# Performance work log

Hardware: AMD Instinct MI355X
Metric: run time of the kernel (lower is better)

Reference implementation:

```python
import jax, jax.numpy as jnp
import numpy as np

B, T, D, FF, H, K = 8, 1024, 512, 2048, 8, 15
HD = D // H  # key_dim = d_model // num_heads


def _ln(x, g, b):
    # keras LayerNormalization default epsilon = 1e-3
    m = jnp.mean(x, axis=-1, keepdims=True)
    v = jnp.var(x, axis=-1, keepdims=True)
    return (x - m) * jax.lax.rsqrt(v + 1e-3) * g + b


def setup_inputs() -> dict:
    key = jax.random.key(0)
    ks = iter(jax.random.split(key, 64))

    def rn(shape, s=0.02):
        return jax.random.normal(next(ks), shape, jnp.float32) * s

    p = {}
    p['x'] = jax.random.normal(next(ks), (B, T, D), jnp.float32)
    # ff_pre: LN -> Dense(FF, relu) -> Dense(D)
    p['g1'] = jnp.ones((D,), jnp.float32); p['b1'] = jnp.zeros((D,), jnp.float32)
    p['Wff1'] = rn((D, FF)); p['bff1'] = jnp.zeros((FF,), jnp.float32)
    p['Wff2'] = rn((FF, D)); p['bff2'] = jnp.zeros((D,), jnp.float32)
    # attention norm + MHA projections (keras EinsumDense shapes)
    p['ga'] = jnp.ones((D,), jnp.float32); p['ba'] = jnp.zeros((D,), jnp.float32)
    p['Wq'] = rn((D, H, HD)); p['bq'] = jnp.zeros((H, HD), jnp.float32)
    p['Wk'] = rn((D, H, HD)); p['bk'] = jnp.zeros((H, HD), jnp.float32)
    p['Wv'] = rn((D, H, HD)); p['bv'] = jnp.zeros((H, HD), jnp.float32)
    p['Wo'] = rn((H, HD, D)); p['bo'] = jnp.zeros((D,), jnp.float32)
    # conv branch: LN -> pointwise conv (2D, gelu) -> depthwise conv(k=15) -> BN -> swish -> pointwise conv (D)
    p['gc'] = jnp.ones((D,), jnp.float32); p['bc'] = jnp.zeros((D,), jnp.float32)
    p['Wcp'] = rn((D, 2 * D)); p['bcp'] = jnp.zeros((2 * D,), jnp.float32)
    p['dwk'] = rn((K, 1, 2 * D)); p['dwb'] = jnp.zeros((2 * D,), jnp.float32)
    p['bn_g'] = jnp.ones((2 * D,), jnp.float32); p['bn_b'] = jnp.zeros((2 * D,), jnp.float32)
    p['bn_m'] = jnp.zeros((2 * D,), jnp.float32)
    p['bn_v'] = jnp.ones((2 * D,), jnp.float32)
    p['Wco'] = rn((2 * D, D)); p['bco'] = jnp.zeros((D,), jnp.float32)
    # ff_post
    p['g2'] = jnp.ones((D,), jnp.float32); p['b2'] = jnp.zeros((D,), jnp.float32)
    p['Wf1'] = rn((D, FF)); p['bf1'] = jnp.zeros((FF,), jnp.float32)
    p['Wf2'] = rn((FF, D)); p['bf2'] = jnp.zeros((D,), jnp.float32)
    return p


def reference(x, g1, b1, Wff1, bff1, Wff2, bff2, ga, ba, Wq, bq, Wk, bk, Wv, bv, Wo, bo, gc, bc, Wcp, bcp, dwk, dwb, bn_g, bn_b, bn_m, bn_v, Wco, bco, g2, b2, Wf1, bf1, Wf2, bf2):
    # Macaron FFN (pre), half-step residual applied later
    x_ff = jnp.maximum(_ln(x, g1, b1) @ Wff1 + bff1, 0.0) @ Wff2 + bff2

    # causal multi-head self-attention (cache=None path)
    a = _ln(x, ga, ba)
    q = jnp.einsum('btd,dhk->bthk', a, Wq) + bq
    k = jnp.einsum('btd,dhk->bthk', a, Wk) + bk
    v = jnp.einsum('btd,dhk->bthk', a, Wv) + bv
    scores = jnp.einsum('bqhd,bkhd->bhqk', q, k) / jnp.sqrt(jnp.float32(HD))
    causal = jnp.tril(jnp.ones((T, T), bool))  # [T,T]
    scores = jnp.where(causal, scores, jnp.float32(-1e9))
    w = jax.nn.softmax(scores, axis=-1)
    ctx = jnp.einsum('bhqk,bkhd->bqhd', w, v)
    attn = jnp.einsum('bqhd,hdo->bqo', ctx, Wo) + bo

    x = x + 0.5 * x_ff + attn

    # convolution module: pointwise(gelu) -> causal left-pad -> depthwise -> BN(inference) -> swish -> pointwise
    c = jax.nn.gelu(_ln(x, gc, bc) @ Wcp + bcp, approximate=False)
    c = jnp.pad(c, ((0, 0), (K - 1, 0), (0, 0)))  # causal pad
    c = jax.lax.conv_general_dilated(
        c, dwk, window_strides=(1,), padding='VALID',
        dimension_numbers=('NWC', 'WIO', 'NWC'), feature_group_count=2 * D) + dwb
    c = (c - bn_m) * jax.lax.rsqrt(bn_v + 1e-3) * bn_g + bn_b
    c = c * jax.nn.sigmoid(c)  # swish
    c = c @ Wco + bco
    x = x + c

    # post FFN (full residual)
    x = x + (jnp.maximum(_ln(x, g2, b2) @ Wf1 + bf1, 0.0) @ Wf2 + bf2)
    return x
```

## Files before the change

kernel.cpp:

```cpp
#include <hip/hip_runtime.h>
#include <hip/hip_bf16.h>
#include <math.h>

#define BB 8
#define TT 1024
#define DD 512
#define FFD 2048
#define HH 8
#define HDD 64
#define KW 15
#define MR (BB*TT)
#define QKVN 1536

typedef __attribute__((ext_vector_type(8))) short short8;
typedef __attribute__((ext_vector_type(4))) short short4v;
typedef __attribute__((ext_vector_type(4))) float f32x4;
typedef __hip_bfloat16 bf16;

__device__ __forceinline__ float bf2f(unsigned u16) {
    return __uint_as_float(u16 << 16);
}

__device__ __forceinline__ void async_copy16(const void* g, void* l) {
    __builtin_amdgcn_global_load_lds(
        (const __attribute__((address_space(1))) void*)g,
        (__attribute__((address_space(3))) void*)l, 16, 0, 0);
}

__device__ __forceinline__ float gelu_exact(float v) {
    return 0.5f * v * (1.0f + erff(v * 0.70710678118654752f));
}

struct PrepPack {
    const float* src[10];
    bf16*        dst[10];
    int          K[10];
    int          lgNT[10];
    float        scale[10];
    int          off[10];
    const float* bq; const float* bk; const float* bv;
    float*       bdst;
    const float* x;
    const float* g1; const float* b1; const float* ga; const float* ba;
    bf16* o1; bf16* o2;
};

__global__ __launch_bounds__(256) void prep_kernel(PrepPack P) {
    __shared__ alignas(16) bf16 T[64][72];
    const int bid = blockIdx.x;
    if (bid == 1536) {
        #pragma unroll
        for (int it = 0; it < 6; ++it) {
            int i = it * 256 + threadIdx.x;
            float v = i < 512 ? P.bq[i] * 0.125f
                              : (i < 1024 ? P.bk[i - 512] : P.bv[i - 1024]);
            P.bdst[i] = v;
        }
        return;
    }
    if (bid > 1536) {
        int wave = ((bid - 1537) * 256 + (int)threadIdx.x) >> 6;
        int lane = threadIdx.x & 63;
        const float* row = P.x + (size_t)wave * DD;
        float4 v0 = ((const float4*)row)[lane];
        float4 v1 = ((const float4*)row)[64 + lane];
        float s  = v0.x + v0.y + v0.z + v0.w + v1.x + v1.y + v1.z + v1.w;
        float ss = v0.x*v0.x + v0.y*v0.y + v0.z*v0.z + v0.w*v0.w
                 + v1.x*v1.x + v1.y*v1.y + v1.z*v1.z + v1.w*v1.w;
        #pragma unroll
        for (int off = 32; off >= 1; off >>= 1) {
            s  += __shfl_xor(s,  off, 64);
            ss += __shfl_xor(ss, off, 64);
        }
        float mean = s * (1.0f / DD);
        float var  = ss * (1.0f / DD) - mean * mean;
        float r    = rsqrtf(var + 1e-3f);
        float n0x = (v0.x - mean) * r, n0y = (v0.y - mean) * r,
              n0z = (v0.z - mean) * r, n0w = (v0.w - mean) * r;
        float n1x = (v1.x - mean) * r, n1y = (v1.y - mean) * r,
              n1z = (v1.z - mean) * r, n1w = (v1.w - mean) * r;
        {
            float4 g0 = ((const float4*)P.g1)[lane];
            float4 gg = ((const float4*)P.g1)[64 + lane];
            float4 b0 = ((const float4*)P.b1)[lane];
            float4 bb = ((const float4*)P.b1)[64 + lane];
            alignas(8) bf16 o0[4], o1[4];
            o0[0] = __float2bfloat16(n0x * g0.x + b0.x);
            o0[1] = __float2bfloat16(n0y * g0.y + b0.y);
            o0[2] = __float2bfloat16(n0z * g0.z + b0.z);
            o0[3] = __float2bfloat16(n0w * g0.w + b0.w);
            o1[0] = __float2bfloat16(n1x * gg.x + bb.x);
            o1[1] = __float2bfloat16(n1y * gg.y + bb.y);
            o1[2] = __float2bfloat16(n1z * gg.z + bb.z);
            o1[3] = __float2bfloat16(n1w * gg.w + bb.w);
            bf16* orow = P.o1 + (size_t)wave * DD;
            *(short4v*)(orow + lane * 4)       = *(const short4v*)o0;
            *(short4v*)(orow + 256 + lane * 4) = *(const short4v*)o1;
        }
        {
            float4 g0 = ((const float4*)P.ga)[lane];
            float4 gg = ((const float4*)P.ga)[64 + lane];
            float4 b0 = ((const float4*)P.ba)[lane];
            float4 bb = ((const float4*)P.ba)[64 + lane];
            alignas(8) bf16 o0[4], o1[4];
            o0[0] = __float2bfloat16(n0x * g0.x + b0.x);
            o0[1] = __float2bfloat16(n0y * g0.y + b0.y);
            o0[2] = __float2bfloat16(n0z * g0.z + b0.z);
            o0[3] = __float2bfloat16(n0w * g0.w + b0.w);
            o1[0] = __float2bfloat16(n1x * gg.x + bb.x);
            o1[1] = __float2bfloat16(n1y * gg.y + bb.y);
            o1[2] = __float2bfloat16(n1z * gg.z + bb.z);
            o1[3] = __float2bfloat16(n1w * gg.w + bb.w);
            bf16* orow = P.o2 + (size_t)wave * DD;
            *(short4v*)(orow + lane * 4)       = *(const short4v*)o0;
            *(short4v*)(orow + 256 + lane * 4) = *(const short4v*)o1;
        }
        return;
    }
    int e = 0;
    #pragma unroll
    for (int i = 1; i < 10; ++i) e = (bid >= P.off[i]) ? i : e;
    const float* W  = P.src[e];
    bf16*        Wt = P.dst[e];
    const int    K  = P.K[e];
    const int    lg = P.lgNT[e];
    const float  scale = P.scale[e];
    const int local = bid - P.off[e];
    const int bx = local & ((1 << lg) - 1);
    const int by = local >> lg;
    const int k0 = by * 64;
    const int n0 = bx * 64;
    const int N  = (1 << lg) * 64;
    const int tid = threadIdx.x;
    #pragma unroll
    for (int it = 0; it < 4; ++it) {
        int lin = it * 256 + tid;
        int kl  = lin >> 4;
        int nq  = (lin & 15) * 4;
        float4 v = *(const float4*)(W + (size_t)(k0 + kl) * N + n0 + nq);
        T[nq + 0][kl] = __float2bfloat16(v.x * scale);
        T[nq + 1][kl] = __float2bfloat16(v.y * scale);
        T[nq + 2][kl] = __float2bfloat16(v.z * scale);
        T[nq + 3][kl] = __float2bfloat16(v.w * scale);
    }
    __syncthreads();
    #pragma unroll
    for (int it = 0; it < 4; ++it) {
        int lin = it * 256 + tid;
        int nl  = lin >> 4;
        int kq  = (lin & 15) * 4;
        *(short4v*)(Wt + (size_t)(n0 + nl) * K + k0 + kq) = *(const short4v*)&T[nl][kq];
    }
}

__global__ __launch_bounds__(256) void ln_kernel(const float* __restrict__ x,
                                                 const float* __restrict__ g,
                                                 const float* __restrict__ b,
                                                 bf16* __restrict__ out) {
    int wave = (blockIdx.x * blockDim.x + threadIdx.x) >> 6;
    int lane = threadIdx.x & 63;
    if (wave >= MR) return;
    const float* row = x + (size_t)wave * DD;
    float4 v0 = ((const float4*)row)[lane];
    float4 v1 = ((const float4*)row)[64 + lane];
    float s  = v0.x + v0.y + v0.z + v0.w + v1.x + v1.y + v1.z + v1.w;
    float ss = v0.x*v0.x + v0.y*v0.y + v0.z*v0.z + v0.w*v0.w
             + v1.x*v1.x + v1.y*v1.y + v1.z*v1.z + v1.w*v1.w;
    #pragma unroll
    for (int off = 32; off >= 1; off >>= 1) {
        s  += __shfl_xor(s,  off, 64);
        ss += __shfl_xor(ss, off, 64);
    }
    float mean = s * (1.0f / DD);
    float var  = ss * (1.0f / DD) - mean * mean;
    float r    = rsqrtf(var + 1e-3f);
    float4 g0 = ((const float4*)g)[lane];
    float4 g1 = ((const float4*)g)[64 + lane];
    float4 b0 = ((const float4*)b)[lane];
    float4 b1 = ((const float4*)b)[64 + lane];
    alignas(8) bf16 o0[4], o1[4];
    o0[0] = __float2bfloat16((v0.x - mean) * r * g0.x + b0.x);
    o0[1] = __float2bfloat16((v0.y - mean) * r * g0.y + b0.y);
    o0[2] = __float2bfloat16((v0.z - mean) * r * g0.z + b0.z);
    o0[3] = __float2bfloat16((v0.w - mean) * r * g0.w + b0.w);
    o1[0] = __float2bfloat16((v1.x - mean) * r * g1.x + b1.x);
    o1[1] = __float2bfloat16((v1.y - mean) * r * g1.y + b1.y);
    o1[2] = __float2bfloat16((v1.z - mean) * r * g1.z + b1.z);
    o1[3] = __float2bfloat16((v1.w - mean) * r * g1.w + b1.w);
    bf16* orow = out + (size_t)wave * DD;
    *(short4v*)(orow + lane * 4)       = *(const short4v*)o0;
    *(short4v*)(orow + 256 + lane * 4) = *(const short4v*)o1;
}

template<int BN, int OP, int RESMODE, int OUTMODE>
__global__ __launch_bounds__(256) void bgemm_kernel(
    const bf16* __restrict__ A,
    const bf16* __restrict__ Bt,
    const float* __restrict__ bias,
    const float* __restrict__ res1,
    const bf16* __restrict__ res2,
    float s2, float oscale,
    void* __restrict__ Cout,
    int N, int Kd, int nxb)
{
    constexpr int NT = BN / 32;
    __shared__ alignas(16) bf16 As[128][64];
    __shared__ alignas(16) bf16 Bs[BN][64];
    const int tid  = threadIdx.x;
    const int w    = tid >> 6;
    const int lane = tid & 63;
    const int quad = lane >> 4;
    const int l16  = lane & 15;
    const int wm   = w >> 1, wn = w & 1;

    const int flat = blockIdx.x;
    const int c8   = flat & 7;
    const int j    = flat >> 3;
    const int jy   = j / nxb;
    const int m0   = (c8 * 8 + jy) * 128;
    const int n0   = (j - jy * nxb) * BN;

    const int srow = lane >> 3;
    const int scol = ((lane & 7) ^ srow) * 8;

    const bf16* Ap = A  + (size_t)(m0 + w * 32 + srow) * Kd + scol;
    const bf16* Bp = Bt + (size_t)(n0 + w * (BN / 4) + srow) * Kd + scol;

    f32x4 acc[4][NT] = {};

    for (int k0 = 0; k0 < Kd; k0 += 64) {
        #pragma unroll
        for (int i = 0; i < 4; ++i)
            async_copy16(Ap + (size_t)(i * 8) * Kd + k0, &As[w * 32 + i * 8][0]);
        #pragma unroll
        for (int i = 0; i < BN / 32; ++i)
            async_copy16(Bp + (size_t)(i * 8) * Kd + k0, &Bs[w * (BN / 4) + i * 8][0]);
        __syncthreads();
        #pragma unroll
        for (int ks = 0; ks < 2; ++ks) {
            short8 af[4], bfr[NT];
            #pragma unroll
            for (int mt = 0; mt < 4; ++mt) {
                const int row = wm * 64 + mt * 16 + l16;
// ... 14 lines not shown
                        af[mt], bfr[nt], acc[mt][nt], 0, 0, 0);
        }
        __syncthreads();
    }

    const int crow0 = m0 + wm * 64 + quad * 4;
    const int ccol0 = n0 + wn * (BN / 2) + l16;
    #pragma unroll
    for (int nt = 0; nt < NT; ++nt) {
        const int col = ccol0 + nt * 16;
        const float bv = bias[col];
        #pragma unroll
        for (int mt = 0; mt < 4; ++mt) {
            #pragma unroll
            for (int r = 0; r < 4; ++r) {
                const int row = crow0 + mt * 16 + r;
                const size_t off = (size_t)row * N + col;
                float o = acc[mt][nt][r] + bv;
                if (OP == 1)      o = fmaxf(o, 0.f);
                else if (OP == 2) o = gelu_exact(o);
                if (RESMODE >= 1) o += res1[off];
                if (RESMODE == 2) o += s2 * __bfloat162float(res2[off]);
                if (OUTMODE == 0) ((float*)Cout)[off] = o;
                else              ((bf16*)Cout)[off]  = __float2bfloat16(o * oscale);
            }
        }
    }
}

__global__ __launch_bounds__(256) void ffqkv_kernel(
    const bf16* __restrict__ lnb, const bf16* __restrict__ lnab,
    const bf16* __restrict__ Wff1t, const bf16* __restrict__ Wqkvt,
    const float* __restrict__ bff1, const float* __restrict__ bqkv,
    bf16* __restrict__ bigb, bf16* __restrict__ qkvb, bf16* __restrict__ Vtb)
{
    __shared__ alignas(16) bf16 As[128][64];
    __shared__ alignas(16) bf16 Bs[128][64];
    const int tid  = threadIdx.x;
    const int w    = tid >> 6;
    const int lane = tid & 63;
    const int quad = lane >> 4;
    const int l16  = lane & 15;
    const int wm   = w >> 1, wn = w & 1;

    const bool jobq = blockIdx.x >= 1024;
    const int  flat = jobq ? (int)blockIdx.x - 1024 : (int)blockIdx.x;
    const int  nxb  = jobq ? 12 : 16;
    const int  N    = jobq ? QKVN : FFD;
    const bf16* A   = jobq ? lnab : lnb;
    const bf16* Bt  = jobq ? Wqkvt : Wff1t;
    const float* bias = jobq ? bqkv : bff1;

    const int c8 = flat & 7;
    const int j  = flat >> 3;
    const int jy = j / nxb;
    const int m0 = (c8 * 8 + jy) * 128;
    const int n0 = (j - jy * nxb) * 128;

    const int srow = lane >> 3;
    const int scol = ((lane & 7) ^ srow) * 8;

    const bf16* Ap = A  + (size_t)(m0 + w * 32 + srow) * DD + scol;
    const bf16* Bp = Bt + (size_t)(n0 + w * 32 + srow) * DD + scol;

    f32x4 acc[4][4] = {};

    for (int k0 = 0; k0 < DD; k0 += 64) {
        #pragma unroll
        for (int i = 0; i < 4; ++i) {
            async_copy16(Ap + (size_t)(i * 8) * DD + k0, &As[w * 32 + i * 8][0]);
            async_copy16(Bp + (size_t)(i * 8) * DD + k0, &Bs[w * 32 + i * 8][0]);
        }
        __syncthreads();
        #pragma unroll
// ... 17 lines not shown
                for (int nt = 0; nt < 4; ++nt)
                    acc[mt][nt] = __builtin_amdgcn_mfma_f32_16x16x32_bf16(
                        af[mt], bfr[nt], acc[mt][nt], 0, 0, 0);
        }
        __syncthreads();
    }

    const int crow0 = m0 + wm * 64 + quad * 4;
    const int ccol0 = n0 + wn * 64 + l16;
    #pragma unroll
    for (int nt = 0; nt < 4; ++nt) {
        const int col = ccol0 + nt * 16;
        const float bv = bias[col];
        #pragma unroll
        for (int mt = 0; mt < 4; ++mt) {
            if (jobq) {
                alignas(8) bf16 o4[4];
                #pragma unroll
                for (int r = 0; r < 4; ++r)
                    o4[r] = __float2bfloat16(acc[mt][nt][r] + bv);
                if (col < 1024) {
                    #pragma unroll
                    for (int r = 0; r < 4; ++r)
                        qkvb[(size_t)(crow0 + mt * 16 + r) * QKVN + col] = o4[r];
                } else {
                    const int dg   = col - 1024;
                    const int rowt = crow0 + mt * 16;
                    const int bb   = rowt >> 10, t0 = rowt & 1023;
                    const int bh2  = bb * 8 + (dg >> 6), d = dg & 63;
                    *(short4v*)(Vtb + ((size_t)bh2 * 64 + d) * TT + t0) =
                        *(const short4v*)o4;
                }
            } else {
                #pragma unroll
                for (int r = 0; r < 4; ++r) {
                    const float o = fmaxf(acc[mt][nt][r] + bv, 0.f);
                    bigb[(size_t)(crow0 + mt * 16 + r) * FFD + col] =
                        __float2bfloat16(o);
                }
            }
        }
    }
}

__global__ __launch_bounds__(256) void ff2attn_kernel(
    const bf16* __restrict__ QKV, const bf16* __restrict__ Vt,
    bf16* __restrict__ ctx,
    const bf16* __restrict__ bigb, const bf16* __restrict__ Wff2t,
    const float* __restrict__ bff2, bf16* __restrict__ xffb)
{
    __shared__ alignas(16) bf16 smem[16384];
    const int tid  = threadIdx.x;
    const int w    = tid >> 6;
    const int lane = tid & 63;
    const int quad = lane >> 4;
    const int l16  = lane & 15;

    if (blockIdx.x < 512) {
        typedef bf16 (*tile_t)[64][64];
        tile_t Ks = (tile_t)smem;
        tile_t Vs = (tile_t)(smem + 2 * 64 * 64);
        const int bh = blockIdx.x & 63;
        const int bi = 7 - ((int)blockIdx.x >> 6);
        const int b = bh >> 3, h = bh & 7;

        const bf16* Qg = QKV + (size_t)(b * TT) * QKVN + h * 64;
        const bf16* Kg = QKV + (size_t)(b * TT) * QKVN + 512 + h * 64;
        const bf16* Vg = Vt  + (size_t)bh * 64 * TT;

        const int qL = bi * 128 + w * 16;
        const int qH = qL + 64;
        short8 qfL0 = *(const short8*)(Qg + (size_t)(qL + l16) * QKVN + quad * 8);
        short8 qfL1 = *(const short8*)(Qg + (size_t)(qL + l16) * QKVN + 32 + quad * 8);
        short8 qfH0 = *(const short8*)(Qg + (size_t)(qH + l16) * QKVN + quad * 8);
        short8 qfH1 = *(const short8*)(Qg + (size_t)(qH + l16) * QKVN + 32 + quad * 8);

        const int sgrow  = lane >> 3;
        const int sgchnk = lane & 7;

        f32x4 caccL[4] = {}, caccH[4] = {};
        float lL = 0.f, lH = 0.f;
        const int prow_base = ((l16 >> 2) << 3) + (l16 & 3);
        const int smax = 2 * bi + 1;

        #pragma unroll
        for (int i = 0; i < 2; ++i) {
            const int rowbase = w * 8 + i * 32;
            const int row = rowbase + sgrow;
            const int fR = (row & 3) | (((row >> 3) & 1) << 2);
            const int sc = sgchnk ^ fR;
            async_copy16(Kg + (size_t)row * QKVN + sc * 8, &Ks[0][rowbase][0]);
// ... 90 lines not shown
            #pragma unroll
            for (int g = 0; g < 4; ++g) {
                const int vrow = g * 16 + l16;
                const int fR = (vrow & 3) | (((vrow >> 3) & 1) << 2);
                short8 va = *(const short8*)&Vs[buf][vrow][(quad ^ fR) * 8];
                short8 vb = *(const short8*)&Vs[buf][vrow][((4 + quad) ^ fR) * 8];
                caccH[g] = __builtin_amdgcn_mfma_f32_16x16x32_bf16(va, pfH0, caccH[g], 0, 0, 0);
                caccH[g] = __builtin_amdgcn_mfma_f32_16x16x32_bf16(vb, pfH1, caccH[g], 0, 0, 0);
                if (doL) {
                    caccL[g] = __builtin_amdgcn_mfma_f32_16x16x32_bf16(va, pfL0, caccL[g], 0, 0, 0);
                    caccL[g] = __builtin_amdgcn_mfma_f32_16x16x32_bf16(vb, pfL1, caccL[g], 0, 0, 0);
                }
            }
            buf ^= 1;
        }

        lL += __shfl_xor(lL, 16, 64);
        lL += __shfl_xor(lL, 32, 64);
        lH += __shfl_xor(lH, 16, 64);
        lH += __shfl_xor(lH, 32, 64);
        const float invL = 1.0f / lL;
        const float invH = 1.0f / lH;

        bf16* CbL = ctx + (size_t)(b * TT + qL + l16) * DD + h * 64;
        bf16* CbH = ctx + (size_t)(b * TT + qH + l16) * DD + h * 64;
        #pragma unroll
        for (int g = 0; g < 4; ++g) {
            alignas(8) bf16 oL[4], oH[4];
            #pragma unroll
            for (int r = 0; r < 4; ++r) {
                oL[r] = __float2bfloat16(caccL[g][r] * invL);
                oH[r] = __float2bfloat16(caccH[g][r] * invH);
            }
            *(short4v*)(CbL + g * 16 + quad * 4) = *(const short4v*)oL;
            *(short4v*)(CbH + g * 16 + quad * 4) = *(const short4v*)oH;
        }
    } else {
        typedef bf16 (*row_t)[64];
        row_t As = (row_t)smem;
        row_t Bs = (row_t)(smem + 128 * 64);
        const int wm = w >> 1, wn = w & 1;

        const int flat = (int)blockIdx.x - 512;
        const int c8 = flat & 7;
        const int j  = flat >> 3;
        const int jy = j >> 3;
        const int m0 = (c8 * 8 + jy) * 128;
        const int n0 = (j & 7) * 64;

        const int srow = lane >> 3;
        const int scol = ((lane & 7) ^ srow) * 8;

        const bf16* Ap = bigb  + (size_t)(m0 + w * 32 + srow) * FFD + scol;
        const bf16* Bp = Wff2t + (size_t)(n0 + w * 16 + srow) * FFD + scol;

        f32x4 acc[4][2] = {};

        for (int k0 = 0; k0 < FFD; k0 += 64) {
            #pragma unroll
            for (int i = 0; i < 4; ++i)
                async_copy16(Ap + (size_t)(i * 8) * FFD + k0, &As[w * 32 + i * 8][0]);
            #pragma unroll
            for (int i = 0; i < 2; ++i)
                async_copy16(Bp + (size_t)(i * 8) * FFD + k0, &Bs[w * 16 + i * 8][0]);
            __syncthreads();
            #pragma unroll
            for (int ks = 0; ks < 2; ++ks) {
                short8 af[4], bfr[2];
                #pragma unroll
                for (int mt = 0; mt < 4; ++mt) {
                    const int row = wm * 64 + mt * 16 + l16;
                    const int c   = ((ks * 4 + quad) ^ (row & 7)) * 16;
                    af[mt] = *(const short8*)((const char*)&As[row][0] + c);
                }
                #pragma unroll
                for (int nt = 0; nt < 2; ++nt) {
                    const int col = wn * 32 + nt * 16 + l16;
                    const int c   = ((ks * 4 + quad) ^ (col & 7)) * 16;
                    bfr[nt] = *(const short8*)((const char*)&Bs[col][0] + c);
                }
                #pragma unroll
                for (int mt = 0; mt < 4; ++mt)
                    #pragma unroll
                    for (int nt = 0; nt < 2; ++nt)
                        acc[mt][nt] = __builtin_amdgcn_mfma_f32_16x16x32_bf16(
                            af[mt], bfr[nt], acc[mt][nt], 0, 0, 0);
            }
            __syncthreads();
        }

        const int crow0 = m0 + wm * 64 + quad * 4;
        const int ccol0 = n0 + wn * 32 + l16;
        #pragma unroll
        for (int nt = 0; nt < 2; ++nt) {
            const int col = ccol0 + nt * 16;
            const float bv = bff2[col];
            #pragma unroll
            for (int mt = 0; mt < 4; ++mt)
                #pragma unroll
                for (int r = 0; r < 4; ++r) {
                    const int row = crow0 + mt * 16 + r;
                    xffb[(size_t)row * DD + col] =
                        __float2bfloat16(acc[mt][nt][r] + bv);
                }
        }
    }
}

__global__ __launch_bounds__(256) void dwconv_kernel(const bf16* __restrict__ c1,
                                                     const float* __restrict__ dwk,
                                                     const float* __restrict__ dwb,
                                                     const float* __restrict__ bn_g,
                                                     const float* __restrict__ bn_b,
                                                     const float* __restrict__ bn_m,
                                                     const float* __restrict__ bn_v,
                                                     bf16* __restrict__ out) {
    const int C2 = 2 * DD;
    const int lin = blockIdx.x * 256 + threadIdx.x;
    const int chp = lin & 511;
    const int ch  = chp << 1;
    const int tch = lin >> 9;
    const int row0 = tch << 3;
    const int t0   = row0 & (TT - 1);

    float w0[KW], w1[KW];
    #pragma unroll
    for (int i = 0; i < KW; ++i) {
        w0[i] = dwk[i * C2 + ch];
        w1[i] = dwk[i * C2 + ch + 1];
    }
    const float a0 = rsqrtf(bn_v[ch] + 1e-3f) * bn_g[ch];
    const float a1 = rsqrtf(bn_v[ch + 1] + 1e-3f) * bn_g[ch + 1];
    const float c0 = (dwb[ch] - bn_m[ch]) * a0 + bn_b[ch];
    const float c1v = (dwb[ch + 1] - bn_m[ch + 1]) * a1 + bn_b[ch + 1];

    float x0[22], x1[22];
    if (t0 >= KW - 1) {
        #pragma unroll
        for (int i = 0; i < 22; ++i) {
            unsigned u = *(const unsigned*)(c1 + (size_t)(row0 - (KW - 1) + i) * C2 + ch);
            x0[i] = bf2f(u & 0xffff);
            x1[i] = bf2f(u >> 16);
        }
    } else {
        #pragma unroll
        for (int i = 0; i < 22; ++i) {
            unsigned u = 0;
            if (t0 - (KW - 1) + i >= 0)
                u = *(const unsigned*)(c1 + (size_t)(row0 - (KW - 1) + i) * C2 + ch);
            x0[i] = bf2f(u & 0xffff);
            x1[i] = bf2f(u >> 16);
        }
    }

    #pragma unroll
    for (int j = 0; j < 8; ++j) {
        float s0 = 0.f, s1 = 0.f;
        #pragma unroll
        for (int i = 0; i < KW; ++i) {
            s0 += x0[j + i] * w0[i];
            s1 += x1[j + i] * w1[i];
        }
        s0 = s0 * a0 + c0;
        s1 = s1 * a1 + c1v;
        s0 = s0 / (1.f + __expf(-s0));
        s1 = s1 / (1.f + __expf(-s1));
        alignas(4) bf16 ob[2] = {__float2bfloat16(s0), __float2bfloat16(s1)};
        *(unsigned*)(out + (size_t)(row0 + j) * C2 + ch) = *(const unsigned*)ob;
    }
}

extern "C" void kernel_launch(void* const* d_in, const int* in_sizes, int n_in,
                              void* d_out, int out_size, void* d_ws, size_t ws_size,
                              hipStream_t stream) {
    const float* x    = (const float*)d_in[0];
    const float* g1   = (const float*)d_in[1];
    const float* b1   = (const float*)d_in[2];
    const float* Wff1 = (const float*)d_in[3];
    const float* bff1 = (const float*)d_in[4];
    const float* Wff2 = (const float*)d_in[5];
    const float* bff2 = (const float*)d_in[6];
    const float* ga   = (const float*)d_in[7];
    const float* ba   = (const float*)d_in[8];
    const float* Wq   = (const float*)d_in[9];
    const float* bq   = (const float*)d_in[10];
    const float* Wk   = (const float*)d_in[11];
    const float* bk   = (const float*)d_in[12];
    const float* Wv   = (const float*)d_in[13];
    const float* bv   = (const float*)d_in[14];
    const float* Wo   = (const float*)d_in[15];
    const float* bo   = (const float*)d_in[16];
    const float* gc   = (const float*)d_in[17];
    const float* bc   = (const float*)d_in[18];
    const float* Wcp  = (const float*)d_in[19];
    const float* bcp  = (const float*)d_in[20];
    const float* dwk  = (const float*)d_in[21];
    const float* dwb  = (const float*)d_in[22];
    const float* bn_g = (const float*)d_in[23];
    const float* bn_b = (const float*)d_in[24];
    const float* bn_m = (const float*)d_in[25];
    const float* bn_v = (const float*)d_in[26];
    const float* Wco  = (const float*)d_in[27];
    const float* bco  = (const float*)d_in[28];
    const float* g2   = (const float*)d_in[29];
    const float* b2   = (const float*)d_in[30];
    const float* Wf1  = (const float*)d_in[31];
    const float* bf1  = (const float*)d_in[32];
    const float* Wf2  = (const float*)d_in[33];
    const float* bf2  = (const float*)d_in[34];

    float* out = (float*)d_out;

    char* p = (char*)d_ws;
    bf16* lnb   = (bf16*)p;  p += (size_t)MR * DD * 2;
    bf16* lnab  = (bf16*)p;  p += (size_t)MR * DD * 2;
    bf16* qkvb  = (bf16*)p;  p += (size_t)MR * QKVN * 2;
    bf16* Vtb   = (bf16*)p;  p += (size_t)MR * DD * 2;
    bf16* ctxb  = (bf16*)p;  p += (size_t)MR * DD * 2;
    bf16* xffb  = (bf16*)p;  p += (size_t)MR * DD * 2;
    bf16* bigb  = (bf16*)p;  p += (size_t)MR * FFD * 2;
    bf16* c2b   = (bf16*)p;  p += (size_t)MR * 1024 * 2;
    bf16* Wff1t = (bf16*)p;  p += (size_t)FFD * DD * 2;
    bf16* Wff2t = (bf16*)p;  p += (size_t)DD * FFD * 2;
    bf16* Wqkvt = (bf16*)p;  p += (size_t)QKVN * DD * 2;
    bf16* Wot   = (bf16*)p;  p += (size_t)DD * DD * 2;
    bf16* Wcpt  = (bf16*)p;  p += (size_t)1024 * DD * 2;
    bf16* Wcot  = (bf16*)p;  p += (size_t)DD * 1024 * 2;
    bf16* Wf1t  = (bf16*)p;  p += (size_t)FFD * DD * 2;
    bf16* Wf2t  = (bf16*)p;  p += (size_t)DD * FFD * 2;
    float* bqkv = (float*)p; p += QKVN * 4;

    dim3 blk(256);

    PrepPack P;
    auto set = [&](int i, const float* s, bf16* d, int K, int N, float sc, int off) {
        P.src[i] = s; P.dst[i] = d; P.K[i] = K; P.scale[i] = sc; P.off[i] = off;
        int nt = N / 64, lg = 0; while ((1 << lg) < nt) ++lg; P.lgNT[i] = lg;
    };
    set(0, Wff1, Wff1t, DD,  FFD, 1.f,    0);
    set(1, Wff2, Wff2t, FFD, DD,  1.f,    256);
    set(2, Wq,   Wqkvt,                DD, DD, 0.125f, 512);
    set(3, Wk,   Wqkvt + (size_t)512 * DD,  DD, DD, 1.f, 576);
    set(4, Wv,   Wqkvt + (size_t)1024 * DD, DD, DD, 1.f, 640);
    set(5, Wo,   Wot,   DD,  DD,  1.f,    704);
    set(6, Wcp,  Wcpt,  DD,  1024, 1.f,   768);
    set(7, Wco,  Wcot,  1024, DD, 1.f,    896);
    set(8, Wf1,  Wf1t,  DD,  FFD, 1.f,    1024);
    set(9, Wf2,  Wf2t,  FFD, DD,  1.f,    1280);
    P.bq = bq; P.bk = bk; P.bv = bv; P.bdst = bqkv;
    P.x = x; P.g1 = g1; P.b1 = b1; P.ga = ga; P.ba = ba;
    P.o1 = lnb; P.o2 = lnab;

    prep_kernel<<<dim3(1537 + MR / 4), blk, 0, stream>>>(P);
    ffqkv_kernel<<<dim3(1024 + 768), blk, 0, stream>>>(
        lnb, lnab, Wff1t, Wqkvt, bff1, bqkv, bigb, qkvb, Vtb);
    ff2attn_kernel<<<dim3(1024), blk, 0, stream>>>(
        qkvb, Vtb, ctxb, bigb, Wff2t, bff2, xffb);
    bgemm_kernel<64, 0, 2, 0><<<dim3(8 * 64), blk, 0, stream>>>(
        ctxb, Wot, bo, x, xffb, 0.5f, 1.f, out, DD, DD, 8);
    ln_kernel<<<dim3(MR / 4), blk, 0, stream>>>(out, gc, bc, lnb);
    bgemm_kernel<128, 2, 0, 1><<<dim3(8 * 64), blk, 0, stream>>>(
        lnb, Wcpt, bcp, nullptr, nullptr, 0.f, 1.f, bigb, 1024, DD, 8);
    dwconv_kernel<<<dim3(MR * 512 / 8 / 256), blk, 0, stream>>>(
        bigb, dwk, dwb, bn_g, bn_b, bn_m, bn_v, c2b);
    bgemm_kernel<64, 0, 1, 0><<<dim3(8 * 64), blk, 0, stream>>>(
        c2b, Wcot, bco, out, nullptr, 0.f, 1.f, out, DD, 1024, 8);
    ln_kernel<<<dim3(MR / 4), blk, 0, stream>>>(out, g2, b2, lnb);
    bgemm_kernel<128, 1, 0, 1><<<dim3(16 * 64), blk, 0, stream>>>(
        lnb, Wf1t, bf1, nullptr, nullptr, 0.f, 1.f, bigb, FFD, DD, 16);
    bgemm_kernel<64, 0, 1, 0><<<dim3(8 * 64), blk, 0, stream>>>(
        bigb, Wf2t, bf2, out, nullptr, 0.f, 1.f, out, DD, FFD, 8);
}
```

Measured before the change: 385.7 us.

## Fuse all stages into one persistent megakernel with software grid barriers

New measurement: 890.9 us. +131.0%, slower.

```diff
diff --git a/kernel.cpp b/kernel.cpp
--- a/kernel.cpp
+++ b/kernel.cpp
@@ -11,6 +11,7 @@
 #define KW 15
 #define MR (BB*TT)
 #define QKVN 1536
+#define NBLK 512
 
 typedef __attribute__((ext_vector_type(8))) short short8;
 typedef __attribute__((ext_vector_type(4))) short short4v;
@@ -31,135 +32,42 @@
     return 0.5f * v * (1.0f + erff(v * 0.70710678118654752f));
 }
 
-struct PrepPack {
-    const float* src[10];
-    bf16*        dst[10];
-    int          K[10];
-    int          lgNT[10];
-    float        scale[10];
-    int          off[10];
-    const float* bq; const float* bk; const float* bv;
-    float*       bdst;
-    const float* x;
-    const float* g1; const float* b1; const float* ga; const float* ba;
-    bf16* o1; bf16* o2;
+__device__ __forceinline__ void grid_barrier(unsigned* cnt, int phase) {
+    __syncthreads();
+    if (threadIdx.x == 0) {
+        __threadfence();
+        atomicAdd(cnt, 1u);
+        const unsigned target = (unsigned)phase * NBLK;
+        while (atomicAdd(cnt, 0u) < target)
+            __builtin_amdgcn_s_sleep(8);
+        __threadfence();
+    }
+    __syncthreads();
+}
+
+struct MegaArgs {
+    const float* wsrc[10];
+    bf16*        wdst[10];
+    int          wK[10];
+    int          wlgNT[10];
+    float        wscale[10];
+    int          woff[10];
+    const float *bq, *bk, *bv;
+    float*       bqkv;
+    const float *x;
+    const float *g1, *b1, *ga, *ba, *gc, *bc, *g2, *b2;
+    const float *bff1, *bff2, *bo, *bcp, *bco, *bf1, *bf2;
+    const float *dwk, *dwb, *bn_g, *bn_b, *bn_m, *bn_v;
+    const bf16 *Wff1t, *Wff2t, *Wqkvt, *Wot, *Wcpt, *Wcot, *Wf1t, *Wf2t;
+    bf16 *lnb, *lnab, *qkvb, *Vtb, *ctxb, *xffb, *bigb, *c2b;
+    float* out;
+    unsigned* bar;
 };
 
-__global__ __launch_bounds__(256) void prep_kernel(PrepPack P) {
-    __shared__ alignas(16) bf16 T[64][72];
-    const int bid = blockIdx.x;
-    if (bid == 1536) {
-        #pragma unroll
-        for (int it = 0; it < 6; ++it) {
-            int i = it * 256 + threadIdx.x;
-            float v = i < 512 ? P.bq[i] * 0.125f
-                              : (i < 1024 ? P.bk[i - 512] : P.bv[i - 1024]);
-            P.bdst[i] = v;
-        }
-        return;
-    }
-    if (bid > 1536) {
-        int wave = ((bid - 1537) * 256 + (int)threadIdx.x) >> 6;
-        int lane = threadIdx.x & 63;
-        const float* row = P.x + (size_t)wave * DD;
-        float4 v0 = ((const float4*)row)[lane];
-        float4 v1 = ((const float4*)row)[64 + lane];
-        float s  = v0.x + v0.y + v0.z + v0.w + v1.x + v1.y + v1.z + v1.w;
-        float ss = v0.x*v0.x + v0.y*v0.y + v0.z*v0.z + v0.w*v0.w
-                 + v1.x*v1.x + v1.y*v1.y + v1.z*v1.z + v1.w*v1.w;
-        #pragma unroll
-        for (int off = 32; off >= 1; off >>= 1) {
-            s  += __shfl_xor(s,  off, 64);
-            ss += __shfl_xor(ss, off, 64);
-        }
-        float mean = s * (1.0f / DD);
-        float var  = ss * (1.0f / DD) - mean * mean;
-        float r    = rsqrtf(var + 1e-3f);
-        float n0x = (v0.x - mean) * r, n0y = (v0.y - mean) * r,
-              n0z = (v0.z - mean) * r, n0w = (v0.w - mean) * r;
-        float n1x = (v1.x - mean) * r, n1y = (v1.y - mean) * r,
-              n1z = (v1.z - mean) * r, n1w = (v1.w - mean) * r;
-        {
-            float4 g0 = ((const float4*)P.g1)[lane];
-            float4 gg = ((const float4*)P.g1)[64 + lane];
-            float4 b0 = ((const float4*)P.b1)[lane];
-            float4 bb = ((const float4*)P.b1)[64 + lane];
-            alignas(8) bf16 o0[4], o1[4];
-            o0[0] = __float2bfloat16(n0x * g0.x + b0.x);
-            o0[1] = __float2bfloat16(n0y * g0.y + b0.y);
-            o0[2] = __float2bfloat16(n0z * g0.z + b0.z);
-            o0[3] = __float2bfloat16(n0w * g0.w + b0.w);
-            o1[0] = __float2bfloat16(n1x * gg.x + bb.x);
-            o1[1] = __float2bfloat16(n1y * gg.y + bb.y);
-            o1[2] = __float2bfloat16(n1z * gg.z + bb.z);
-            o1[3] = __float2bfloat16(n1w * gg.w + bb.w);
-            bf16* orow = P.o1 + (size_t)wave * DD;
-            *(short4v*)(orow + lane * 4)       = *(const short4v*)o0;
-            *(short4v*)(orow + 256 + lane * 4) = *(const short4v*)o1;
-        }
-        {
-            float4 g0 = ((const float4*)P.ga)[lane];
-            float4 gg = ((const float4*)P.ga)[64 + lane];
-            float4 b0 = ((const float4*)P.ba)[lane];
-            float4 bb = ((const float4*)P.ba)[64 + lane];
-            alignas(8) bf16 o0[4], o1[4];
-            o0[0] = __float2bfloat16(n0x * g0.x + b0.x);
-            o0[1] = __float2bfloat16(n0y * g0.y + b0.y);
-            o0[2] = __float2bfloat16(n0z * g0.z + b0.z);
-            o0[3] = __float2bfloat16(n0w * g0.w + b0.w);
-            o1[0] = __float2bfloat16(n1x * gg.x + bb.x);
-            o1[1] = __float2bfloat16(n1y * gg.y + bb.y);
-            o1[2] = __float2bfloat16(n1z * gg.z + bb.z);
-            o1[3] = __float2bfloat16(n1w * gg.w + bb.w);
-            bf16* orow = P.o2 + (size_t)wave * DD;
-            *(short4v*)(orow + lane * 4)       = *(const short4v*)o0;
-            *(short4v*)(orow + 256 + lane * 4) = *(const short4v*)o1;
-        }
-        return;
-    }
-    int e = 0;
-    #pragma unroll
-    for (int i = 1; i < 10; ++i) e = (bid >= P.off[i]) ? i : e;
-    const float* W  = P.src[e];
-    bf16*        Wt = P.dst[e];
-    const int    K  = P.K[e];
-    const int    lg = P.lgNT[e];
-    const float  scale = P.scale[e];
-    const int local = bid - P.off[e];
-    const int bx = local & ((1 << lg) - 1);
-    const int by = local >> lg;
-    const int k0 = by * 64;
-    const int n0 = bx * 64;
-    const int N  = (1 << lg) * 64;
-    const int tid = threadIdx.x;
-    #pragma unroll
-    for (int it = 0; it < 4; ++it) {
-        int lin = it * 256 + tid;
-        int kl  = lin >> 4;
-        int nq  = (lin & 15) * 4;
-        float4 v = *(const float4*)(W + (size_t)(k0 + kl) * N + n0 + nq);
-        T[nq + 0][kl] = __float2bfloat16(v.x * scale);
-        T[nq + 1][kl] = __float2bfloat16(v.y * scale);
-        T[nq + 2][kl] = __float2bfloat16(v.z * scale);
-        T[nq + 3][kl] = __float2bfloat16(v.w * scale);
-    }
-    __syncthreads();
-    #pragma unroll
-    for (int it = 0; it < 4; ++it) {
-        int lin = it * 256 + tid;
-        int nl  = lin >> 4;
-        int kq  = (lin & 15) * 4;
-        *(short4v*)(Wt + (size_t)(n0 + nl) * K + k0 + kq) = *(const short4v*)&T[nl][kq];
-    }
-}
-
-__global__ __launch_bounds__(256) void ln_kernel(const float* __restrict__ x,
-                                                 const float* __restrict__ g,
-                                                 const float* __restrict__ b,
-                                                 bf16* __restrict__ out) {
-    int wave = (blockIdx.x * blockDim.x + threadIdx.x) >> 6;
+__device__ __forceinline__ void dev_ln(int job, const float* x, const float* g,
+                                       const float* b, bf16* out) {
+    int wave = (job * 256 + (int)threadIdx.x) >> 6;
     int lane = threadIdx.x & 63;
-    if (wave >= MR) return;
     const float* row = x + (size_t)wave * DD;
     float4 v0 = ((const float4*)row)[lane];
     float4 v1 = ((const float4*)row)[64 + lane];
@@ -192,20 +100,124 @@
     *(short4v*)(orow + 256 + lane * 4) = *(const short4v*)o1;
 }
 
+__device__ __forceinline__ void dev_prep(int bid, const MegaArgs& A, bf16* smem) {
+    if (bid == 1536) {
+        #pragma unroll
+        for (int it = 0; it < 6; ++it) {
+            int i = it * 256 + threadIdx.x;
+            float v = i < 512 ? A.bq[i] * 0.125f
+                              : (i < 1024 ? A.bk[i - 512] : A.bv[i - 1024]);
+            A.bqkv[i] = v;
+        }
+        return;
+    }
+    if (bid > 1536) {
+        int wave = ((bid - 1537) * 256 + (int)threadIdx.x) >> 6;
+        int lane = threadIdx.x & 63;
+        const float* row = A.x + (size_t)wave * DD;
+        float4 v0 = ((const float4*)row)[lane];
+        float4 v1 = ((const float4*)row)[64 + lane];
+        float s  = v0.x + v0.y + v0.z + v0.w + v1.x + v1.y + v1.z + v1.w;
+        float ss = v0.x*v0.x + v0.y*v0.y + v0.z*v0.z + v0.w*v0.w
+                 + v1.x*v1.x + v1.y*v1.y + v1.z*v1.z + v1.w*v1.w;
+        #pragma unroll
+        for (int off = 32; off >= 1; off >>= 1) {
+            s  += __shfl_xor(s,  off, 64);
+            ss += __shfl_xor(ss, off, 64);
+        }
+        float mean = s * (1.0f / DD);
+        float var  = ss * (1.0f / DD) - mean * mean;
+        float r    = rsqrtf(var + 1e-3f);
+        float n0x = (v0.x - mean) * r, n0y = (v0.y - mean) * r,
+              n0z = (v0.z - mean) * r, n0w = (v0.w - mean) * r;
+        float n1x = (v1.x - mean) * r, n1y = (v1.y - mean) * r,
+              n1z = (v1.z - mean) * r, n1w = (v1.w - mean) * r;
+        {
+            float4 g0 = ((const float4*)A.g1)[lane];
+            float4 gg = ((const float4*)A.g1)[64 + lane];
+            float4 b0 = ((const float4*)A.b1)[lane];
+            float4 bb = ((const float4*)A.b1)[64 + lane];
+            alignas(8) bf16 o0[4], o1[4];
+            o0[0] = __float2bfloat16(n0x * g0.x + b0.x);
+            o0[1] = __float2bfloat16(n0y * g0.y + b0.y);
+            o0[2] = __float2bfloat16(n0z * g0.z + b0.z);
+            o0[3] = __float2bfloat16(n0w * g0.w + b0.w);
+            o1[0] = __float2bfloat16(n1x * gg.x + bb.x);
+            o1[1] = __float2bfloat16(n1y * gg.y + bb.y);
+            o1[2] = __float2bfloat16(n1z * gg.z + bb.z);
+            o1[3] = __float2bfloat16(n1w * gg.w + bb.w);
+            bf16* orow = A.lnb + (size_t)wave * DD;
+            *(short4v*)(orow + lane * 4)       = *(const short4v*)o0;
+            *(short4v*)(orow + 256 + lane * 4) = *(const short4v*)o1;
+        }
+        {
+            float4 g0 = ((const float4*)A.ga)[lane];
+            float4 gg = ((const float4*)A.ga)[64 + lane];
+            float4 b0 = ((const float4*)A.ba)[lane];
+            float4 bb = ((const float4*)A.ba)[64 + lane];
+            alignas(8) bf16 o0[4], o1[4];
+            o0[0] = __float2bfloat16(n0x * g0.x + b0.x);
+            o0[1] = __float2bfloat16(n0y * g0.y + b0.y);
+            o0[2] = __float2bfloat16(n0z * g0.z + b0.z);
+            o0[3] = __float2bfloat16(n0w * g0.w + b0.w);
+            o1[0] = __float2bfloat16(n1x * gg.x + bb.x);
+            o1[1] = __float2bfloat16(n1y * gg.y + bb.y);
+            o1[2] = __float2bfloat16(n1z * gg.z + bb.z);
+            o1[3] = __float2bfloat16(n1w * gg.w + bb.w);
+            bf16* orow = A.lnab + (size_t)wave * DD;
+            *(short4v*)(orow + lane * 4)       = *(const short4v*)o0;
+            *(short4v*)(orow + 256 + lane * 4) = *(const short4v*)o1;
+        }
+        return;
+    }
+    bf16 (*T)[72] = (bf16(*)[72])smem;
+    int e = 0;
+    #pragma unroll
+    for (int i = 1; i < 10; ++i) e = (bid >= A.woff[i]) ? i : e;
+    const float* W  = A.wsrc[e];
+    bf16*        Wt = A.wdst[e];
+    const int    K  = A.wK[e];
+    const int    lg = A.wlgNT[e];
+    const float  scale = A.wscale[e];
+    const int local = bid - A.woff[e];
+    const int bx = local & ((1 << lg) - 1);
+    const int by = local >> lg;
+    const int k0 = by * 64;
+    const int n0 = bx * 64;
+    const int N  = (1 << lg) * 64;
+    const int tid = threadIdx.x;
+    #pragma unroll
+    for (int it = 0; it < 4; ++it) {
+        int lin = it * 256 + tid;
+        int kl  = lin >> 4;
+        int nq  = (lin & 15) * 4;
+        float4 v = *(const float4*)(W + (size_t)(k0 + kl) * N + n0 + nq);
+        T[nq + 0][kl] = __float2bfloat16(v.x * scale);
+        T[nq + 1][kl] = __float2bfloat16(v.y * scale);
+        T[nq + 2][kl] = __float2bfloat16(v.z * scale);
+        T[nq + 3][kl] = __float2bfloat16(v.w * scale);
+    }
+    __syncthreads();
+    #pragma unroll
+    for (int it = 0; it < 4; ++it) {
+        int lin = it * 256 + tid;
+        int nl  = lin >> 4;
+        int kq  = (lin & 15) * 4;
+        *(short4v*)(Wt + (size_t)(n0 + nl) * K + k0 + kq) = *(const short4v*)&T[nl][kq];
+    }
+    __syncthreads();
+}
+
 template<int BN, int OP, int RESMODE, int OUTMODE>
-__global__ __launch_bounds__(256) void bgemm_kernel(
-    const bf16* __restrict__ A,
-    const bf16* __restrict__ Bt,
-    const float* __restrict__ bias,
-    const float* __restrict__ res1,
-    const bf16* __restrict__ res2,
-    float s2, float oscale,
-    void* __restrict__ Cout,
+__device__ __forceinline__ void dev_gemm(int flat, bf16* smem,
+    const bf16* __restrict__ A, const bf16* __restrict__ Bt,
+    const float* __restrict__ bias, const float* __restrict__ res1,
+    const bf16* __restrict__ res2, float s2, void* __restrict__ Cout,
     int N, int Kd, int nxb)
 {
     constexpr int NT = BN / 32;
-    __shared__ alignas(16) bf16 As[128][64];
-    __shared__ alignas(16) bf16 Bs[BN][64];
+    bf16 (*As)[64] = (bf16(*)[64])smem;
+    bf16 (*Bs)[64] = (bf16(*)[64])(smem + 128 * 64);
     const int tid  = threadIdx.x;
     const int w    = tid >> 6;
     const int lane = tid & 63;
@@ -213,12 +225,11 @@
     const int l16  = lane & 15;
     const int wm   = w >> 1, wn = w & 1;
 
-    const int flat = blockIdx.x;
-    const int c8   = flat & 7;
-    const int j    = flat >> 3;
-    const int jy   = j / nxb;
-    const int m0   = (c8 * 8 + jy) * 128;
-    const int n0   = (j - jy * nxb) * BN;
+    const int c8 = flat & 7;
+    const int j  = flat >> 3;
+    const int jy = j / nxb;
+    const int m0 = (c8 * 8 + jy) * 128;
+    const int n0 = (j - jy * nxb) * BN;
 
     const int srow = lane >> 3;
     const int scol = ((lane & 7) ^ srow) * 8;
@@ -279,20 +290,15 @@
                 if (RESMODE >= 1) o += res1[off];
                 if (RESMODE == 2) o += s2 * __bfloat162float(res2[off]);
                 if (OUTMODE == 0) ((float*)Cout)[off] = o;
-                else              ((bf16*)Cout)[off]  = __float2bfloat16(o * oscale);
-            }
-        }
-    }
-}
-
-__global__ __launch_bounds__(256) void ffqkv_kernel(
-    const bf16* __restrict__ lnb, const bf16* __restrict__ lnab,
-    const bf16* __restrict__ Wff1t, const bf16* __restrict__ Wqkvt,
-    const float* __restrict__ bff1, const float* __restrict__ bqkv,
-    bf16* __restrict__ bigb, bf16* __restrict__ qkvb, bf16* __restrict__ Vtb)
-{
-    __shared__ alignas(16) bf16 As[128][64];
-    __shared__ alignas(16) bf16 Bs[128][64];
+                else              ((bf16*)Cout)[off]  = __float2bfloat16(o);
+            }
+        }
+    }
+}
+
+__device__ __forceinline__ void dev_ffqkv(int job, bf16* smem, const MegaArgs& Ar) {
+    bf16 (*As)[64] = (bf16(*)[64])smem;
+    bf16 (*Bs)[64] = (bf16(*)[64])(smem + 128 * 64);
     const int tid  = threadIdx.x;
     const int w    = tid >> 6;
     const int lane = tid & 63;
@@ -300,13 +306,13 @@
     const int l16  = lane & 15;
     const int wm   = w >> 1, wn = w & 1;
 
-    const bool jobq = blockIdx.x >= 1024;
-    const int  flat = jobq ? (int)blockIdx.x - 1024 : (int)blockIdx.x;
+    const bool jobq = job >= 1024;
+    const int  flat = jobq ? job - 1024 : job;
     const int  nxb  = jobq ? 12 : 16;
     const int  N    = jobq ? QKVN : FFD;
-    const bf16* A   = jobq ? lnab : lnb;
-    const bf16* Bt  = jobq ? Wqkvt : Wff1t;
-    const float* bias = jobq ? bqkv : bff1;
+    const bf16* A   = jobq ? Ar.lnab : Ar.lnb;
+    const bf16* Bt  = jobq ? Ar.Wqkvt : Ar.Wff1t;
+    const float* bias = jobq ? Ar.bqkv : Ar.bff1;
 
     const int c8 = flat & 7;
     const int j  = flat >> 3;
@@ -370,20 +376,20 @@
                 if (col < 1024) {
                     #pragma unroll
                     for (int r = 0; r < 4; ++r)
-                        qkvb[(size_t)(crow0 + mt * 16 + r) * QKVN + col] = o4[r];
+                        Ar.qkvb[(size_t)(crow0 + mt * 16 + r) * QKVN + col] = o4[r];
                 } else {
                     const int dg   = col - 1024;
                     const int rowt = crow0 + mt * 16;
                     const int bb   = rowt >> 10, t0 = rowt & 1023;
                     const int bh2  = bb * 8 + (dg >> 6), d = dg & 63;
-                    *(short4v*)(Vtb + ((size_t)bh2 * 64 + d) * TT + t0) =
+                    *(short4v*)(Ar.Vtb + ((size_t)bh2 * 64 + d) * TT + t0) =
                         *(const short4v*)o4;
                 }
             } else {
                 #pragma unroll
                 for (int r = 0; r < 4; ++r) {
                     const float o = fmaxf(acc[mt][nt][r] + bv, 0.f);
-                    bigb[(size_t)(crow0 + mt * 16 + r) * FFD + col] =
+                    Ar.bigb[(size_t)(crow0 + mt * 16 + r) * FFD + col] =
                         __float2bfloat16(o);
                 }
             }
@@ -391,30 +397,24 @@
     }
 }
 
-__global__ __launch_bounds__(256) void ff2attn_kernel(
-    const bf16* __restrict__ QKV, const bf16* __restrict__ Vt,
-    bf16* __restrict__ ctx,
-    const bf16* __restrict__ bigb, const bf16* __restrict__ Wff2t,
-    const float* __restrict__ bff2, bf16* __restrict__ xffb)
-{
-    __shared__ alignas(16) bf16 smem[16384];
+__device__ __forceinline__ void dev_ff2attn(int job, bf16* smem, const MegaArgs& Ar) {
     const int tid  = threadIdx.x;
     const int w    = tid >> 6;
     const int lane = tid & 63;
     const int quad = lane >> 4;
     const int l16  = lane & 15;
 
-    if (blockIdx.x < 512) {
+    if (job < 512) {
         typedef bf16 (*tile_t)[64][64];
         tile_t Ks = (tile_t)smem;
         tile_t Vs = (tile_t)(smem + 2 * 64 * 64);
-        const int bh = blockIdx.x & 63;
-        const int bi = 7 - ((int)blockIdx.x >> 6);
+        const int bh = job & 63;
+        const int bi = 7 - (job >> 6);
         const int b = bh >> 3, h = bh & 7;
 
-        const bf16* Qg = QKV + (size_t)(b * TT) * QKVN + h * 64;
-        const bf16* Kg = QKV + (size_t)(b * TT) * QKVN + 512 + h * 64;
-        const bf16* Vg = Vt  + (size_t)bh * 64 * TT;
+        const bf16* Qg = Ar.qkvb + (size_t)(b * TT) * QKVN + h * 64;
+        const bf16* Kg = Ar.qkvb + (size_t)(b * TT) * QKVN + 512 + h * 64;
+        const bf16* Vg = Ar.Vtb  + (size_t)bh * 64 * TT;
 
         const int qL = bi * 128 + w * 16;
         const int qH = qL + 64;
@@ -551,8 +551,8 @@
         const float invL = 1.0f / lL;
         const float invH = 1.0f / lH;
 
-        bf16* CbL = ctx + (size_t)(b * TT + qL + l16) * DD + h * 64;
-        bf16* CbH = ctx + (size_t)(b * TT + qH + l16) * DD + h * 64;
+        bf16* CbL = Ar.ctxb + (size_t)(b * TT + qL + l16) * DD + h * 64;
+        bf16* CbH = Ar.ctxb + (size_t)(b * TT + qH + l16) * DD + h * 64;
         #pragma unroll
         for (int g = 0; g < 4; ++g) {
             alignas(8) bf16 oL[4], oH[4];
@@ -564,13 +564,13 @@
             *(short4v*)(CbL + g * 16 + quad * 4) = *(const short4v*)oL;
             *(short4v*)(CbH + g * 16 + quad * 4) = *(const short4v*)oH;
         }
+        __syncthreads();
     } else {
-        typedef bf16 (*row_t)[64];
-        row_t As = (row_t)smem;
-        row_t Bs = (row_t)(smem + 128 * 64);
+        bf16 (*As)[64] = (bf16(*)[64])smem;
+        bf16 (*Bs)[64] = (bf16(*)[64])(smem + 128 * 64);
         const int wm = w >> 1, wn = w & 1;
 
-        const int flat = (int)blockIdx.x - 512;
+        const int flat = job - 512;
         const int c8 = flat & 7;
         const int j  = flat >> 3;
         const int jy = j >> 3;
@@ -580,8 +580,8 @@
         const int srow = lane >> 3;
         const int scol = ((lane & 7) ^ srow) * 8;
 
-        const bf16* Ap = bigb  + (size_t)(m0 + w * 32 + srow) * FFD + scol;
-        const bf16* Bp = Wff2t + (size_t)(n0 + w * 16 + srow) * FFD + scol;
+        const bf16* Ap = Ar.bigb  + (size_t)(m0 + w * 32 + srow) * FFD + scol;
+        const bf16* Bp = Ar.Wff2t + (size_t)(n0 + w * 16 + srow) * FFD + scol;
 
         f32x4 acc[4][2] = {};
 
@@ -623,45 +623,39 @@
         #pragma unroll
         for (int nt = 0; nt < 2; ++nt) {
             const int col = ccol0 + nt * 16;
-            const float bv = bff2[col];
+            const float bv = Ar.bff2[col];
             #pragma unroll
             for (int mt = 0; mt < 4; ++mt)
                 #pragma unroll
                 for (int r = 0; r < 4; ++r) {
                     const int row = crow0 + mt * 16 + r;
-                    xffb[(size_t)row * DD + col] =
+                    Ar.xffb[(size_t)row * DD + col] =
                         __float2bfloat16(acc[mt][nt][r] + bv);
                 }
         }
     }
 }
 
-__global__ __launch_bounds__(256) void dwconv_kernel(const bf16* __restrict__ c1,
-                                                     const float* __restrict__ dwk,
-                                                     const float* __restrict__ dwb,
-                                                     const float* __restrict__ bn_g,
-                                                     const float* __restrict__ bn_b,
-                                                     const float* __restrict__ bn_m,
-                                                     const float* __restrict__ bn_v,
-                                                     bf16* __restrict__ out) {
+__device__ __forceinline__ void dev_dwconv(int job, const MegaArgs& A) {
     const int C2 = 2 * DD;
-    const int lin = blockIdx.x * 256 + threadIdx.x;
+    const int lin = job * 256 + threadIdx.x;
     const int chp = lin & 511;
     const int ch  = chp << 1;
     const int tch = lin >> 9;
     const int row0 = tch << 3;
     const int t0   = row0 & (TT - 1);
+    const bf16* c1 = A.bigb;
 
     float w0[KW], w1[KW];
     #pragma unroll
     for (int i = 0; i < KW; ++i) {
-        w0[i] = dwk[i * C2 + ch];
-        w1[i] = dwk[i * C2 + ch + 1];
-    }
-    const float a0 = rsqrtf(bn_v[ch] + 1e-3f) * bn_g[ch];
-    const float a1 = rsqrtf(bn_v[ch + 1] + 1e-3f) * bn_g[ch + 1];
-    const float c0 = (dwb[ch] - bn_m[ch]) * a0 + bn_b[ch];
-    const float c1v = (dwb[ch + 1] - bn_m[ch + 1]) * a1 + bn_b[ch + 1];
+        w0[i] = A.dwk[i * C2 + ch];
+        w1[i] = A.dwk[i * C2 + ch + 1];
+    }
+    const float a0 = rsqrtf(A.bn_v[ch] + 1e-3f) * A.bn_g[ch];
+    const float a1 = rsqrtf(A.bn_v[ch + 1] + 1e-3f) * A.bn_g[ch + 1];
+    const float c0 = (A.dwb[ch] - A.bn_m[ch]) * a0 + A.bn_b[ch];
+    const float c1v = (A.dwb[ch + 1] - A.bn_m[ch + 1]) * a1 + A.bn_b[ch + 1];
 
     float x0[22], x1[22];
     if (t0 >= KW - 1) {
@@ -683,20 +677,53 @@
     }
 
     #pragma unroll
-    for (int j = 0; j < 8; ++j) {
+    for (int jj = 0; jj < 8; ++jj) {
         float s0 = 0.f, s1 = 0.f;
         #pragma unroll
         for (int i = 0; i < KW; ++i) {
-            s0 += x0[j + i] * w0[i];
-            s1 += x1[j + i] * w1[i];
+            s0 += x0[jj + i] * w0[i];
+            s1 += x1[jj + i] * w1[i];
         }
         s0 = s0 * a0 + c0;
         s1 = s1 * a1 + c1v;
         s0 = s0 / (1.f + __expf(-s0));
         s1 = s1 / (1.f + __expf(-s1));
         alignas(4) bf16 ob[2] = {__float2bfloat16(s0), __float2bfloat16(s1)};
-        *(unsigned*)(out + (size_t)(row0 + j) * C2 + ch) = *(const unsigned*)ob;
-    }
+        *(unsigned*)(A.c2b + (size_t)(row0 + jj) * C2 + ch) = *(const unsigned*)ob;
+    }
+}
+
+__global__ __launch_bounds__(256, 2) void mega_kernel(MegaArgs A) {
+    __shared__ alignas(16) bf16 smem[16384];
+    const int blk = blockIdx.x;
+
+    for (int job = blk; job < 3585; job += NBLK) dev_prep(job, A, smem);
+    grid_barrier(A.bar, 1);
+    for (int job = blk; job < 1792; job += NBLK) dev_ffqkv(job, smem, A);
+    grid_barrier(A.bar, 2);
+    for (int job = blk; job < 1024; job += NBLK) dev_ff2attn(job, smem, A);
+    grid_barrier(A.bar, 3);
+    dev_gemm<64, 0, 2, 0>(blk, smem, A.ctxb, A.Wot, A.bo, A.x, A.xffb, 0.5f,
+                          A.out, DD, DD, 8);
+    grid_barrier(A.bar, 4);
+    for (int job = blk; job < 2048; job += NBLK) dev_ln(job, A.out, A.gc, A.bc, A.lnb);
+    grid_barrier(A.bar, 5);
+    dev_gemm<128, 2, 0, 1>(blk, smem, A.lnb, A.Wcpt, A.bcp, nullptr, nullptr, 0.f,
+                           A.bigb, 1024, DD, 8);
+    grid_barrier(A.bar, 6);
+    for (int job = blk; job < 2048; job += NBLK) dev_dwconv(job, A);
+    grid_barrier(A.bar, 7);
+    dev_gemm<64, 0, 1, 0>(blk, smem, A.c2b, A.Wcot, A.bco, A.out, nullptr, 0.f,
+                          A.out, DD, 1024, 8);
+    grid_barrier(A.bar, 8);
+    for (int job = blk; job < 2048; job += NBLK) dev_ln(job, A.out, A.g2, A.b2, A.lnb);
+    grid_barrier(A.bar, 9);
+    for (int job = blk; job < 1024; job += NBLK)
+        dev_gemm<128, 1, 0, 1>(job, smem, A.lnb, A.Wf1t, A.bf1, nullptr, nullptr, 0.f,
+                               A.bigb, FFD, DD, 16);
+    grid_barrier(A.bar, 10);
+    dev_gemm<64, 0, 1, 0>(blk, smem, A.bigb, A.Wf2t, A.bf2, A.out, nullptr, 0.f,
+                          A.out, DD, FFD, 8);
 }
 
 extern "C" void kernel_launch(void* const* d_in, const int* in_sizes, int n_in,
@@ -738,8 +765,6 @@
     const float* Wf2  = (const float*)d_in[33];
     const float* bf2  = (const float*)d_in[34];
 
-    float* out = (float*)d_out;
-
     char* p = (char*)d_ws;
     bf16* lnb   = (bf16*)p;  p += (size_t)MR * DD * 2;
     bf16* lnab  = (bf16*)p;  p += (size_t)MR * DD * 2;
@@ -758,13 +783,12 @@
     bf16* Wf1t  = (bf16*)p;  p += (size_t)FFD * DD * 2;
     bf16* Wf2t  = (bf16*)p;  p += (size_t)DD * FFD * 2;
     float* bqkv = (float*)p; p += QKVN * 4;
-
-    dim3 blk(256);
-
-    PrepPack P;
+    unsigned* bar = (unsigned*)p; p += 256;
+
+    MegaArgs A;
     auto set = [&](int i, const float* s, bf16* d, int K, int N, float sc, int off) {
-        P.src[i] = s; P.dst[i] = d; P.K[i] = K; P.scale[i] = sc; P.off[i] = off;
-        int nt = N / 64, lg = 0; while ((1 << lg) < nt) ++lg; P.lgNT[i] = lg;
+        A.wsrc[i] = s; A.wdst[i] = d; A.wK[i] = K; A.wscale[i] = sc; A.woff[i] = off;
+        int nt = N / 64, lg = 0; while ((1 << lg) < nt) ++lg; A.wlgNT[i] = lg;
     };
     set(0, Wff1, Wff1t, DD,  FFD, 1.f,    0);
     set(1, Wff2, Wff2t, FFD, DD,  1.f,    256);
@@ -776,27 +800,21 @@
     set(7, Wco,  Wcot,  1024, DD, 1.f,    896);
     set(8, Wf1,  Wf1t,  DD,  FFD, 1.f,    1024);
     set(9, Wf2,  Wf2t,  FFD, DD,  1.f,    1280);
-    P.bq = bq; P.bk = bk; P.bv = bv; P.bdst = bqkv;
-    P.x = x; P.g1 = g1; P.b1 = b1; P.ga = ga; P.ba = ba;
-    P.o1 = lnb; P.o2 = lnab;
-
-    prep_kernel<<<dim3(1537 + MR / 4), blk, 0, stream>>>(P);
-    ffqkv_kernel<<<dim3(1024 + 768), blk, 0, stream>>>(
-        lnb, lnab, Wff1t, Wqkvt, bff1, bqkv, bigb, qkvb, Vtb);
-    ff2attn_kernel<<<dim3(1024), blk, 0, stream>>>(
-        qkvb, Vtb, ctxb, bigb, Wff2t, bff2, xffb);
-    bgemm_kernel<64, 0, 2, 0><<<dim3(8 * 64), blk, 0, stream>>>(
-        ctxb, Wot, bo, x, xffb, 0.5f, 1.f, out, DD, DD, 8);
-    ln_kernel<<<dim3(MR / 4), blk, 0, stream>>>(out, gc, bc, lnb);
-    bgemm_kernel<128, 2, 0, 1><<<dim3(8 * 64), blk, 0, stream>>>(
-        lnb, Wcpt, bcp, nullptr, nullptr, 0.f, 1.f, bigb, 1024, DD, 8);
-    dwconv_kernel<<<dim3(MR * 512 / 8 / 256), blk, 0, stream>>>(
-        bigb, dwk, dwb, bn_g, bn_b, bn_m, bn_v, c2b);
-    bgemm_kernel<64, 0, 1, 0><<<dim3(8 * 64), blk, 0, stream>>>(
-        c2b, Wcot, bco, out, nullptr, 0.f, 1.f, out, DD, 1024, 8);
-    ln_kernel<<<dim3(MR / 4), blk, 0, stream>>>(out, g2, b2, lnb);
-    bgemm_kernel<128, 1, 0, 1><<<dim3(16 * 64), blk, 0, stream>>>(
-        lnb, Wf1t, bf1, nullptr, nullptr, 0.f, 1.f, bigb, FFD, DD, 16);
-    bgemm_kernel<64, 0, 1, 0><<<dim3(8 * 64), blk, 0, stream>>>(
-        bigb, Wf2t, bf2, out, nullptr, 0.f, 1.f, out, DD, FFD, 8);
-}
+    A.bq = bq; A.bk = bk; A.bv = bv; A.bqkv = bqkv;
+    A.x = x;
+    A.g1 = g1; A.b1 = b1; A.ga = ga; A.ba = ba;
+    A.gc = gc; A.bc = bc; A.g2 = g2; A.b2 = b2;
+    A.bff1 = bff1; A.bff2 = bff2; A.bo = bo; A.bcp = bcp; A.bco = bco;
+    A.bf1 = bf1; A.bf2 = bf2;
+    A.dwk = dwk; A.dwb = dwb; A.bn_g = bn_g; A.bn_b = bn_b;
+    A.bn_m = bn_m; A.bn_v = bn_v;
+    A.Wff1t = Wff1t; A.Wff2t = Wff2t; A.Wqkvt = Wqkvt; A.Wot = Wot;
+    A.Wcpt = Wcpt; A.Wcot = Wcot; A.Wf1t = Wf1t; A.Wf2t = Wf2t;
+    A.lnb = lnb; A.lnab = lnab; A.qkvb = qkvb; A.Vtb = Vtb; A.ctxb = ctxb;
+    A.xffb = xffb; A.bigb = bigb; A.c2b = c2b;
+    A.out = (float*)d_out;
+    A.bar = bar;
+
+    hipMemsetAsync(bar, 0, 256, stream);
+    mega_kernel<<<dim3(NBLK), dim3(256), 0, stream>>>(A);
+}
```
